# Kernel optimization log

Measured on AMD Instinct MI355X. Metric: run time of the kernel, lower is better.

The kernel has to match this reference:

```python
import jax, jax.numpy as jnp
import numpy as np

N_HEAD = 12
NEG_INF = -10000.0


def setup_inputs() -> dict:
    key = jax.random.key(0)
    k1, k2, k3 = jax.random.split(key, 3)
    B, S, D = 8, 1024, 768
    std = 0.01
    return {
        "hidden_states": jax.random.normal(k1, (B, S, D), dtype=jnp.float32),
        "Wqkv": jax.random.normal(k2, (D, 3 * D), dtype=jnp.float32) * std,
        "bqkv": jnp.zeros((3 * D,), dtype=jnp.float32),
        "Wout": jax.random.normal(k3, (D, D), dtype=jnp.float32) * std,
        "bout": jnp.zeros((D,), dtype=jnp.float32),
    }


def reference(hidden_states, Wqkv, bqkv, Wout, bout):
    B, S, D = hidden_states.shape
    H = N_HEAD
    hd = D // H
    # fused QKV projection
    qkv = hidden_states @ Wqkv + bqkv  # [B,S,3D]
    qkv = qkv.reshape(B, S, 3, H, hd)
    q, k, v = qkv[:, :, 0], qkv[:, :, 1], qkv[:, :, 2]  # [B,S,H,hd]
    q = q.transpose(0, 2, 1, 3)  # [B,H,S,hd]
    k = k.transpose(0, 2, 1, 3)
    v = v.transpose(0, 2, 1, 3)
    scale = 1.0 / jnp.sqrt(jnp.asarray(hd, dtype=hidden_states.dtype))
    scores = jnp.einsum("bhqd,bhkd->bhqk", q, k) * scale  # [B,H,S,S]
    causal = jnp.tril(jnp.ones((S, S), dtype=bool))[None, None]
    scores = jnp.where(causal, scores, jnp.asarray(NEG_INF, scores.dtype))
    probs = jax.nn.softmax(scores, axis=-1)
    # dropout is identity in eval/deterministic mode
    attn = jnp.einsum("bhqk,bhkd->bhqd", probs, v)  # [B,H,S,hd]
    attn = attn.transpose(0, 2, 1, 3).reshape(B, S, D)
    return attn @ Wout + bout
```

## Files before the change

kernel.cpp:

```cpp
#include <hip/hip_runtime.h>
#include <hip/hip_bf16.h>

#define B_   8
#define S_   1024
#define D_   768
#define H_   12
#define HD_  64
#define BS_  (B_*S_)
#define N3_  (3*D_)

typedef __attribute__((ext_vector_type(8))) short short8;
typedef __attribute__((ext_vector_type(4))) float f32x4;

__device__ __forceinline__ short8 ld8(const __hip_bfloat16* p) {
    return *reinterpret_cast<const short8*>(p);
}
__device__ __forceinline__ void st8(__hip_bfloat16* p, short8 v) {
    *reinterpret_cast<short8*>(p) = v;
}
__device__ __forceinline__ f32x4 mfma16(short8 a, short8 b, f32x4 c) {
    return __builtin_amdgcn_mfma_f32_16x16x32_bf16(a, b, c, 0, 0, 0);
}
__device__ __forceinline__ void async16(const __hip_bfloat16* g, __hip_bfloat16* l) {
    __builtin_amdgcn_global_load_lds((const __attribute__((address_space(1))) void*)g,
                                     (__attribute__((address_space(3))) void*)l,
                                     16, 0, 0);
}
__device__ __forceinline__ float fast_exp2(float x) {
#if __has_builtin(__builtin_amdgcn_exp2f)
    return __builtin_amdgcn_exp2f(x);
#else
    return __expf(x * 0.69314718056f);
#endif
}

#define PREP_CAST_BLK 6144
#define PREP_WQKV_BLK 1728
#define PREP_WOUT_BLK 576
__global__ __launch_bounds__(256)
void prep(const float* __restrict__ X, __hip_bfloat16* __restrict__ Xbf,
          const float* __restrict__ Wqkv, __hip_bfloat16* __restrict__ WqkvT,
          const float* __restrict__ Wout, __hip_bfloat16* __restrict__ WoutT) {
    __shared__ float tile[32][33];
    int b = blockIdx.x, tid = threadIdx.x;
    if (b < PREP_CAST_BLK) {
        int i = (b * 256 + tid) * 4;
        float4 v = *reinterpret_cast<const float4*>(X + i);
        __hip_bfloat16 tmp[4];
        tmp[0] = __float2bfloat16(v.x);
        tmp[1] = __float2bfloat16(v.y);
        tmp[2] = __float2bfloat16(v.z);
        tmp[3] = __float2bfloat16(v.w);
        *reinterpret_cast<ushort4*>(Xbf + i) =
            *reinterpret_cast<const ushort4*>(tmp);
        return;
    }
    const float* in; __hip_bfloat16* out; int Rr, Cc, bx, by;
    if (b < PREP_CAST_BLK + PREP_WQKV_BLK) {
        int sub = b - PREP_CAST_BLK;
        bx = sub % (N3_ / 32); by = sub / (N3_ / 32);
        in = Wqkv; out = WqkvT; Rr = D_; Cc = N3_;
    } else {
        int sub = b - PREP_CAST_BLK - PREP_WQKV_BLK;
        bx = sub % (D_ / 32); by = sub / (D_ / 32);
        in = Wout; out = WoutT; Rr = D_; Cc = D_;
    }
    int tx = tid & 31, ty = tid >> 5;
    int c0 = bx * 32, r0 = by * 32;
    for (int i = ty; i < 32; i += 8)
        tile[i][tx] = in[(size_t)(r0 + i) * Cc + c0 + tx];
    __syncthreads();
    for (int i = ty; i < 32; i += 8)
        out[(size_t)(c0 + i) * Rr + r0 + tx] = __float2bfloat16(tile[tx][i]);
}

__global__ __launch_bounds__(256)
void gemm_qkv(const __hip_bfloat16* __restrict__ A,
              const __hip_bfloat16* __restrict__ Bt,
              const float* __restrict__ bqkv,
              __hip_bfloat16* __restrict__ Qb,
              __hip_bfloat16* __restrict__ Kb,
              __hip_bfloat16* __restrict__ Vtb) {
    __shared__ __align__(16) char smem[49152];
    __hip_bfloat16* Ct = (__hip_bfloat16*)smem;

    int tid = threadIdx.x, wave = tid >> 6, lane = tid & 63;
    int ln = lane & 15, quad = lane >> 4;
    int lin = blockIdx.y * 18 + blockIdx.x;
    int work = (lin & 7) * 144 + (lin >> 3);
    int mbb = work / 18, nbb = work % 18;
    int mb = mbb * 128, nb = nbb * 128;
    int wm = (wave >> 1) * 64, wn = (wave & 1) * 64;

    f32x4 acc[4][4];
#pragma unroll
    for (int i = 0; i < 4; ++i)
#pragma unroll
        for (int j = 0; j < 4; ++j) acc[i][j] = (f32x4){0.f, 0.f, 0.f, 0.f};

    auto stage = [&](int k, int bufoff) {
        __hip_bfloat16* Asb = (__hip_bfloat16*)(smem + bufoff);
        __hip_bfloat16* Bsb = Asb + 128 * 32;
#pragma unroll
        for (int it = 0; it < 2; ++it) {
            int c = it * 256 + tid;
            int row = c >> 2, cc = c & 3;
            int csw = cc ^ ((row >> 1) & 3);
            async16(A + (size_t)(mb + row) * D_ + k + csw * 8,
                    Asb + it * 2048 + wave * 512);
            async16(Bt + (size_t)(nb + row) * D_ + k + csw * 8,
                    Bsb + it * 2048 + wave * 512);
        }
    };

    auto compute = [&](int bufoff) {
        __hip_bfloat16* As = (__hip_bfloat16*)(smem + bufoff);
        __hip_bfloat16* Bs = As + 128 * 32;
        short8 a[4], b[4];
#pragma unroll
        for (int i = 0; i < 4; ++i) {
            int row = wm + i * 16 + ln;
            a[i] = ld8(As + row * 32 + ((quad ^ ((row >> 1) & 3)) << 3));
        }
#pragma unroll
        for (int j = 0; j < 4; ++j) {
            int row = wn + j * 16 + ln;
            b[j] = ld8(Bs + row * 32 + ((quad ^ ((row >> 1) & 3)) << 3));
        }
#pragma unroll
        for (int i = 0; i < 4; ++i)
#pragma unroll
            for (int j = 0; j < 4; ++j)
                acc[i][j] = mfma16(a[i], b[j], acc[i][j]);
    };

    stage(0, 0);
    stage(32, 16384);
    int cb = 0;
    for (int k = 0; k < D_ - 32; k += 32) {
        asm volatile("s_waitcnt vmcnt(4)" ::: "memory");
        asm volatile("s_barrier" ::: "memory");
        if (k + 64 < D_) {
            int sb = cb + 32768; if (sb >= 49152) sb -= 49152;
            stage(k + 64, sb);
        }
        compute(cb);
        cb += 16384; if (cb >= 49152) cb = 0;
    }
    asm volatile("s_waitcnt vmcnt(0)" ::: "memory");
    asm volatile("s_barrier" ::: "memory");
    compute(cb);
    __syncthreads();

    int which = nbb / 6;
    int nbr = nb - which * D_;
    float qscale = (which == 0) ? (0.125f * 1.44269504089f) : 1.f;

#pragma unroll
    for (int j = 0; j < 4; ++j) {
        int col = wn + j * 16 + ln;
        float bias = bqkv[nb + col];
#pragma unroll
        for (int i = 0; i < 4; ++i)
#pragma unroll
            for (int r = 0; r < 4; ++r) {
                int row = wm + i * 16 + quad * 4 + r;
                __hip_bfloat16 v = __float2bfloat16((acc[i][j][r] + bias) * qscale);
                if (which != 2) Ct[row * 132 + col] = v;
                else            Ct[col * 132 + row] = v;
            }
    }
    __syncthreads();

    int bb = mb >> 10, sb = mb & 1023;
    if (which != 2) {
        __hip_bfloat16* dst = (which == 0) ? Qb : Kb;
#pragma unroll
        for (int it = 0; it < 8; ++it) {
            int cc = it * 256 + tid;
            int row = cc >> 4, c8 = cc & 15;
            short8 v = ld8(Ct + row * 132 + c8 * 8);
            int gcol = nbr + c8 * 8;
            int h = gcol >> 6, d = gcol & 63;
            int s = sb + row;
            st8(dst + (((size_t)(bb * H_ + h)) * S_ + s) * HD_ + d, v);
        }
    } else {
#pragma unroll
        for (int it = 0; it < 8; ++it) {
            int cc = it * 256 + tid;
            int drow = cc >> 4, s8 = cc & 15;
            short8 v = ld8(Ct + drow * 132 + s8 * 8);
            int gd = nbr + drow;
            int h = gd >> 6, d = gd & 63;
            st8(Vtb + ((size_t)(bb * H_ + h) * HD_ + d) * S_ + sb + s8 * 8, v);
        }
    }
}

__global__ __launch_bounds__(256, 3)
void attn_flash3(const __hip_bfloat16* __restrict__ Q,
                 const __hip_bfloat16* __restrict__ K,
                 const __hip_bfloat16* __restrict__ Vt,
                 __hip_bfloat16* __restrict__ attnbf) {
    __shared__ __hip_bfloat16 Kbuf[2][64 * 64];
    __shared__ __hip_bfloat16 Vbuf[2][64 * 64];
    __shared__ __hip_bfloat16 Pbuf[4][32 * 72];

    int tid = threadIdx.x;
    int wave = tid >> 6, lane = tid & 63;
    int ln = lane & 15, quad = lane >> 4;

    int lin = blockIdx.y * 8 + blockIdx.x;
    int xcd = lin & 7;
    int idx = lin >> 3;
    int jj  = idx & 7;
    int bh  = (idx >> 3) * 8 + xcd;
    int r   = idx >> 5;

    const int TBL1[8] = {4, 5, 6, 7, 0, 1, 2, 3};
    const int TBL2[8] = {6, 4, 2, 0, 7, 5, 3, 1};
    int jp = (r == 0) ? jj : (r == 1) ? TBL1[jj] : TBL2[jj];
    int strip = jp * 2 + (wave >> 1);
    int qrow0 = strip * 64 + (wave & 1) * 32;
    int last_kt = jp * 2 + 1;

    const __hip_bfloat16* Qbh = Q + (size_t)bh * S_ * HD_;
    const __hip_bfloat16* Kbh = K + (size_t)bh * S_ * HD_;
    const __hip_bfloat16* Vbh = Vt + (size_t)bh * HD_ * S_;

    short8 aq[2][2];
#pragma unroll
    for (int rt = 0; rt < 2; ++rt)
#pragma unroll
        for (int ks = 0; ks < 2; ++ks)
            aq[rt][ks] = ld8(Qbh + (size_t)(qrow0 + rt * 16 + ln) * HD_ +
                             ks * 32 + quad * 8);

    f32x4 o[2][4];
    float l_run[2][4];
#pragma unroll
    for (int rt = 0; rt < 2; ++rt)
#pragma unroll
        for (int n = 0; n < 4; ++n) {
            o[rt][n] = (f32x4){0.f, 0.f, 0.f, 0.f};
            l_run[rt][n] = 0.f;
        }

    auto stage = [&](int kt, int buf) {
        const __hip_bfloat16* gK = Kbh + (size_t)kt * 64 * HD_;
#pragma unroll
        for (int it = 0; it < 2; ++it) {
            int p = it * 256 + tid;
            int row = p >> 3;
            int csw = (p & 7) ^ (row & 7);
            async16(gK + row * HD_ + csw * 8,
                    &Kbuf[buf][it * 2048 + wave * 512]);
            async16(Vbh + (size_t)row * S_ + kt * 64 + csw * 8,
                    &Vbuf[buf][it * 2048 + wave * 512]);
        }
    };

    stage(0, 0);
    __syncthreads();
    int cur = 0;

    for (int kt = 0; kt <= last_kt; ++kt) {
        int kbase = kt * 64;
        if (kt < last_kt) stage(kt + 1, cur ^ 1);

        if (kbase <= qrow0 + 31) {
            const __hip_bfloat16* Kc = Kbuf[cur];
            const __hip_bfloat16* Vc = Vbuf[cur];

            f32x4 s[2][4];
#pragma unroll
            for (int rt = 0; rt < 2; ++rt)
#pragma unroll
                for (int j = 0; j < 4; ++j) s[rt][j] = (f32x4){0.f, 0.f, 0.f, 0.f};
            __builtin_amdgcn_s_setprio(1);
#pragma unroll
            for (int j = 0; j < 4; ++j) {
                int row = j * 16 + ln;
#pragma unroll
                for (int ks = 0; ks < 2; ++ks) {
                    short8 bk = ld8(&Kc[row * 64 +
                                        (((ks * 4 + quad) ^ (row & 7)) << 3)]);
#pragma unroll
                    for (int rt = 0; rt < 2; ++rt)
                        s[rt][j] = mfma16(aq[rt][ks], bk, s[rt][j]);
                }
            }
            __builtin_amdgcn_s_setprio(0);

            if (kbase + 63 > qrow0) {
#pragma unroll
                for (int rt = 0; rt < 2; ++rt)
#pragma unroll
                    for (int j = 0; j < 4; ++j) {
                        int key = kbase + j * 16 + ln;
#pragma unroll
                        for (int r2 = 0; r2 < 4; ++r2) {
                            int q = qrow0 + rt * 16 + quad * 4 + r2;
                            if (key > q) s[rt][j][r2] = -INFINITY;
                        }
                    }
            }

#pragma unroll
            for (int rt = 0; rt < 2; ++rt)
#pragma unroll
                for (int j = 0; j < 4; ++j)
#pragma unroll
                    for (int r2 = 0; r2 < 4; ++r2)
                        s[rt][j][r2] = fast_exp2(s[rt][j][r2]);
#pragma unroll
            for (int rt = 0; rt < 2; ++rt)
#pragma unroll
                for (int r2 = 0; r2 < 4; ++r2)
                    l_run[rt][r2] += (s[rt][0][r2] + s[rt][1][r2]) +
                                     (s[rt][2][r2] + s[rt][3][r2]);

#pragma unroll
            for (int rt = 0; rt < 2; ++rt)
#pragma unroll
                for (int j = 0; j < 4; ++j)
#pragma unroll
                    for (int r2 = 0; r2 < 4; ++r2)
                        Pbuf[wave][(rt * 16 + quad * 4 + r2) * 72 + j * 16 + ln] =
                            __float2bfloat16(s[rt][j][r2]);

            short8 ap[2][2];
            asm volatile("s_waitcnt lgkmcnt(15)" ::: "memory");
            __builtin_amdgcn_sched_barrier(0);
#pragma unroll
            for (int ks = 0; ks < 2; ++ks)
                ap[0][ks] = ld8(&Pbuf[wave][(0 * 16 + ln) * 72 +
                                            ks * 32 + quad * 8]);
            asm volatile("s_waitcnt lgkmcnt(0)" ::: "memory");
            __builtin_amdgcn_sched_barrier(0);
#pragma unroll
            for (int ks = 0; ks < 2; ++ks)
                ap[1][ks] = ld8(&Pbuf[wave][(1 * 16 + ln) * 72 +
                                            ks * 32 + quad * 8]);

            __builtin_amdgcn_s_setprio(1);
#pragma unroll
            for (int n = 0; n < 4; ++n) {
                int row = n * 16 + ln;
#pragma unroll
                for (int ks = 0; ks < 2; ++ks) {
                    short8 bv = ld8(&Vc[row * 64 +
                                        (((ks * 4 + quad) ^ (row & 7)) << 3)]);
#pragma unroll
                    for (int rt = 0; rt < 2; ++rt)
                        o[rt][n] = mfma16(ap[rt][ks], bv, o[rt][n]);
                }
            }
            __builtin_amdgcn_s_setprio(0);
        }

        __syncthreads();
        cur ^= 1;
    }

    int bb = bh / H_, h = bh - bb * H_;
#pragma unroll
    for (int rt = 0; rt < 2; ++rt)
#pragma unroll
        for (int r2 = 0; r2 < 4; ++r2) {
            float l = l_run[rt][r2];
            l += __shfl_xor(l, 1);
            l += __shfl_xor(l, 2);
            l += __shfl_xor(l, 4);
            l += __shfl_xor(l, 8);
            float inv = 1.f / l;
            int row = qrow0 + rt * 16 + quad * 4 + r2;
#pragma unroll
            for (int n = 0; n < 4; ++n) {
                int col = h * 64 + n * 16 + ln;
                attnbf[((size_t)bb * S_ + row) * D_ + col] =
                    __float2bfloat16(o[rt][n][r2] * inv);
            }
        }
}

__global__ __launch_bounds__(256, 4)
void gemm_out(const __hip_bfloat16* __restrict__ A,
              const __hip_bfloat16* __restrict__ Bt,
              const float* __restrict__ bias,
              float* __restrict__ Cout) {
    __shared__ __align__(16) char smem[36864];

    int tid = threadIdx.x, wave = tid >> 6, lane = tid & 63;
    int ln = lane & 15, quad = lane >> 4;
    int lin = blockIdx.y * 12 + blockIdx.x;
    int work = (lin & 7) * 96 + (lin >> 3);
    int mbb = work / 12, nbb = work % 12;
    int mb = mbb * 128, nb = nbb * 64;
    int wm = (wave >> 1) * 64, wn = (wave & 1) * 32;

    f32x4 acc[4][2];
#pragma unroll
    for (int i = 0; i < 4; ++i)
#pragma unroll
        for (int j = 0; j < 2; ++j) acc[i][j] = (f32x4){0.f, 0.f, 0.f, 0.f};

    auto stage = [&](int k, int bufoff) {
        __hip_bfloat16* Asb = (__hip_bfloat16*)(smem + bufoff);
        __hip_bfloat16* Bsb = Asb + 128 * 32;
#pragma unroll
        for (int it = 0; it < 2; ++it) {
            int c = it * 256 + tid;
            int row = c >> 2, cc = c & 3;
            int csw = cc ^ ((row >> 1) & 3);
            async16(A + (size_t)(mb + row) * D_ + k + csw * 8,
                    Asb + it * 2048 + wave * 512);
        }
        {
            int c = tid;
            int row = c >> 2, cc = c & 3;
            int csw = cc ^ ((row >> 1) & 3);
            async16(Bt + (size_t)(nb + row) * D_ + k + csw * 8,
                    Bsb + wave * 512);
        }
    };

    auto compute = [&](int bufoff) {
        __hip_bfloat16* As = (__hip_bfloat16*)(smem + bufoff);
        __hip_bfloat16* Bs = As + 128 * 32;
        short8 a[4], b[2];
#pragma unroll
        for (int i = 0; i < 4; ++i) {
            int row = wm + i * 16 + ln;
            a[i] = ld8(As + row * 32 + ((quad ^ ((row >> 1) & 3)) << 3));
        }
#pragma unroll
        for (int j = 0; j < 2; ++j) {
            int row = wn + j * 16 + ln;
            b[j] = ld8(Bs + row * 32 + ((quad ^ ((row >> 1) & 3)) << 3));
        }
#pragma unroll
        for (int i = 0; i < 4; ++i)
#pragma unroll
            for (int j = 0; j < 2; ++j)
                acc[i][j] = mfma16(a[i], b[j], acc[i][j]);
    };

    stage(0, 0);
    stage(32, 12288);
    int cb = 0;
    for (int k = 0; k < D_ - 32; k += 32) {
        asm volatile("s_waitcnt vmcnt(3)" ::: "memory");
        asm volatile("s_barrier" ::: "memory");
        if (k + 64 < D_) {
            int sb = cb + 24576; if (sb >= 36864) sb -= 36864;
            stage(k + 64, sb);
        }
        compute(cb);
        cb += 12288; if (cb >= 36864) cb = 0;
    }
    asm volatile("s_waitcnt vmcnt(0)" ::: "memory");
    asm volatile("s_barrier" ::: "memory");
    compute(cb);

#pragma unroll
    for (int j = 0; j < 2; ++j) {
        int col = nb + wn + j * 16 + ln;
        float bv = bias[col];
#pragma unroll
        for (int i = 0; i < 4; ++i)
#pragma unroll
            for (int r = 0; r < 4; ++r) {
                int row = mb + wm + i * 16 + quad * 4 + r;
                Cout[(size_t)row * D_ + col] = acc[i][j][r] + bv;
            }
    }
}

extern "C" void kernel_launch(void* const* d_in, const int* in_sizes, int n_in,
                              void* d_out, int out_size, void* d_ws, size_t ws_size,
                              hipStream_t stream) {
    const float* X    = (const float*)d_in[0];
    const float* Wqkv = (const float*)d_in[1];
    const float* bqkv = (const float*)d_in[2];
    const float* Wout = (const float*)d_in[3];
    const float* bout = (const float*)d_in[4];
    float* out = (float*)d_out;

    constexpr size_t SZ_XBF   = (size_t)BS_ * D_ * 2;
    constexpr size_t SZ_WQKVT = (size_t)N3_ * D_ * 2;
    constexpr size_t SZ_WOUTT = (size_t)D_ * D_ * 2;
    constexpr size_t SZ_QKV   = (size_t)B_ * H_ * S_ * HD_ * 2;

    char* w = (char*)d_ws;
    __hip_bfloat16* Xbf    = (__hip_bfloat16*)(w);
    __hip_bfloat16* WqkvT  = (__hip_bfloat16*)(w + SZ_XBF);
    __hip_bfloat16* WoutT  = (__hip_bfloat16*)(w + SZ_XBF + SZ_WQKVT);
    __hip_bfloat16* Qb     = (__hip_bfloat16*)(w + SZ_XBF + SZ_WQKVT + SZ_WOUTT);
    __hip_bfloat16* Kb     = (__hip_bfloat16*)(w + SZ_XBF + SZ_WQKVT + SZ_WOUTT + SZ_QKV);
    __hip_bfloat16* Vtb    = (__hip_bfloat16*)(w + SZ_XBF + SZ_WQKVT + SZ_WOUTT + 2*SZ_QKV);
    __hip_bfloat16* attnbf = (__hip_bfloat16*)(w + SZ_XBF + SZ_WQKVT + SZ_WOUTT + 3*SZ_QKV);
    (void)ws_size; (void)in_sizes; (void)n_in; (void)out_size;

    prep<<<PREP_CAST_BLK + PREP_WQKV_BLK + PREP_WOUT_BLK, 256, 0, stream>>>(
        X, Xbf, Wqkv, WqkvT, Wout, WoutT);

    gemm_qkv<<<dim3(N3_ / 128, BS_ / 128), 256, 0, stream>>>(Xbf, WqkvT, bqkv, Qb, Kb, Vtb);

    attn_flash3<<<dim3(8, B_ * H_), 256, 0, stream>>>(Qb, Kb, Vtb, attnbf);

    gemm_out<<<dim3(D_ / 64, BS_ / 128), 256, 0, stream>>>(attnbf, WoutT, bout, out);
}
```

Before: 178.9 us.

## Restructure QKV GEMM into single-wave 64x128 tiles with triple-buffered loads

```diff
diff --git a/kernel.cpp b/kernel.cpp
--- a/kernel.cpp
+++ b/kernel.cpp
@@ -74,110 +74,111 @@
         out[(size_t)(c0 + i) * Rr + r0 + tx] = __float2bfloat16(tile[tx][i]);
 }
 
-__global__ __launch_bounds__(256)
+__global__ __launch_bounds__(64)
 void gemm_qkv(const __hip_bfloat16* __restrict__ A,
               const __hip_bfloat16* __restrict__ Bt,
               const float* __restrict__ bqkv,
               __hip_bfloat16* __restrict__ Qb,
               __hip_bfloat16* __restrict__ Kb,
               __hip_bfloat16* __restrict__ Vtb) {
-    __shared__ __align__(16) char smem[49152];
+    __shared__ __align__(16) char smem[36864];
     __hip_bfloat16* Ct = (__hip_bfloat16*)smem;
 
-    int tid = threadIdx.x, wave = tid >> 6, lane = tid & 63;
+    int lane = threadIdx.x;
     int ln = lane & 15, quad = lane >> 4;
     int lin = blockIdx.y * 18 + blockIdx.x;
-    int work = (lin & 7) * 144 + (lin >> 3);
+    int work = (lin & 7) * 288 + (lin >> 3);
     int mbb = work / 18, nbb = work % 18;
-    int mb = mbb * 128, nb = nbb * 128;
-    int wm = (wave >> 1) * 64, wn = (wave & 1) * 64;
-
-    f32x4 acc[4][4];
+    int mb = mbb * 64, nb = nbb * 128;
+
+    f32x4 acc[4][8];
 #pragma unroll
     for (int i = 0; i < 4; ++i)
 #pragma unroll
-        for (int j = 0; j < 4; ++j) acc[i][j] = (f32x4){0.f, 0.f, 0.f, 0.f};
+        for (int j = 0; j < 8; ++j) acc[i][j] = (f32x4){0.f, 0.f, 0.f, 0.f};
 
     auto stage = [&](int k, int bufoff) {
         __hip_bfloat16* Asb = (__hip_bfloat16*)(smem + bufoff);
-        __hip_bfloat16* Bsb = Asb + 128 * 32;
-#pragma unroll
-        for (int it = 0; it < 2; ++it) {
-            int c = it * 256 + tid;
-            int row = c >> 2, cc = c & 3;
+        __hip_bfloat16* Bsb = Asb + 64 * 32;
+#pragma unroll
+        for (int ld = 0; ld < 4; ++ld) {
+            int q = ld * 64 + lane;
+            int row = q >> 2, cc = q & 3;
             int csw = cc ^ ((row >> 1) & 3);
             async16(A + (size_t)(mb + row) * D_ + k + csw * 8,
-                    Asb + it * 2048 + wave * 512);
+                    Asb + ld * 512);
+        }
+#pragma unroll
+        for (int ld = 0; ld < 8; ++ld) {
+            int q = ld * 64 + lane;
+            int row = q >> 2, cc = q & 3;
+            int csw = cc ^ ((row >> 1) & 3);
             async16(Bt + (size_t)(nb + row) * D_ + k + csw * 8,
-                    Bsb + it * 2048 + wave * 512);
+                    Bsb + ld * 512);
         }
     };
 
     auto compute = [&](int bufoff) {
         __hip_bfloat16* As = (__hip_bfloat16*)(smem + bufoff);
-        __hip_bfloat16* Bs = As + 128 * 32;
-        short8 a[4], b[4];
+        __hip_bfloat16* Bs = As + 64 * 32;
+        short8 a[4], b[8];
 #pragma unroll
         for (int i = 0; i < 4; ++i) {
-            int row = wm + i * 16 + ln;
+            int row = i * 16 + ln;
             a[i] = ld8(As + row * 32 + ((quad ^ ((row >> 1) & 3)) << 3));
         }
 #pragma unroll
-        for (int j = 0; j < 4; ++j) {
-            int row = wn + j * 16 + ln;
+        for (int j = 0; j < 8; ++j) {
+            int row = j * 16 + ln;
             b[j] = ld8(Bs + row * 32 + ((quad ^ ((row >> 1) & 3)) << 3));
         }
 #pragma unroll
         for (int i = 0; i < 4; ++i)
 #pragma unroll
-            for (int j = 0; j < 4; ++j)
+            for (int j = 0; j < 8; ++j)
                 acc[i][j] = mfma16(a[i], b[j], acc[i][j]);
     };
 
     stage(0, 0);
-    stage(32, 16384);
-    int cb = 0;
-    for (int k = 0; k < D_ - 32; k += 32) {
-        asm volatile("s_waitcnt vmcnt(4)" ::: "memory");
-        asm volatile("s_barrier" ::: "memory");
-        if (k + 64 < D_) {
-            int sb = cb + 32768; if (sb >= 49152) sb -= 49152;
-            stage(k + 64, sb);
-        }
-        compute(cb);
-        cb += 16384; if (cb >= 49152) cb = 0;
-    }
-    asm volatile("s_waitcnt vmcnt(0)" ::: "memory");
-    asm volatile("s_barrier" ::: "memory");
-    compute(cb);
-    __syncthreads();
+    stage(32, 12288);
+    for (int t = 0; t < 24; ++t) {
+        if (t < 23) {
+            asm volatile("s_waitcnt vmcnt(12)" ::: "memory");
+        } else {
+            asm volatile("s_waitcnt vmcnt(0)" ::: "memory");
+        }
+        if (t + 2 < 24) {
+            int sb = (t + 2) % 3;
+            stage((t + 2) * 32, sb * 12288);
+        }
+        compute((t % 3) * 12288);
+    }
 
     int which = nbb / 6;
     int nbr = nb - which * D_;
     float qscale = (which == 0) ? (0.125f * 1.44269504089f) : 1.f;
 
 #pragma unroll
-    for (int j = 0; j < 4; ++j) {
-        int col = wn + j * 16 + ln;
+    for (int j = 0; j < 8; ++j) {
+        int col = j * 16 + ln;
         float bias = bqkv[nb + col];
 #pragma unroll
         for (int i = 0; i < 4; ++i)
 #pragma unroll
             for (int r = 0; r < 4; ++r) {
-                int row = wm + i * 16 + quad * 4 + r;
+                int row = i * 16 + quad * 4 + r;
                 __hip_bfloat16 v = __float2bfloat16((acc[i][j][r] + bias) * qscale);
                 if (which != 2) Ct[row * 132 + col] = v;
-                else            Ct[col * 132 + row] = v;
+                else            Ct[col * 68 + row] = v;
             }
     }
-    __syncthreads();
 
     int bb = mb >> 10, sb = mb & 1023;
     if (which != 2) {
         __hip_bfloat16* dst = (which == 0) ? Qb : Kb;
 #pragma unroll
-        for (int it = 0; it < 8; ++it) {
-            int cc = it * 256 + tid;
+        for (int it = 0; it < 16; ++it) {
+            int cc = it * 64 + lane;
             int row = cc >> 4, c8 = cc & 15;
             short8 v = ld8(Ct + row * 132 + c8 * 8);
             int gcol = nbr + c8 * 8;
@@ -187,10 +188,10 @@
         }
     } else {
 #pragma unroll
-        for (int it = 0; it < 8; ++it) {
-            int cc = it * 256 + tid;
-            int drow = cc >> 4, s8 = cc & 15;
-            short8 v = ld8(Ct + drow * 132 + s8 * 8);
+        for (int it = 0; it < 16; ++it) {
+            int cc = it * 64 + lane;
+            int drow = cc >> 3, s8 = cc & 7;
+            short8 v = ld8(Ct + drow * 68 + s8 * 8);
             int gd = nbr + drow;
             int h = gd >> 6, d = gd & 63;
             st8(Vtb + ((size_t)(bb * H_ + h) * HD_ + d) * S_ + sb + s8 * 8, v);
@@ -506,7 +507,7 @@
     prep<<<PREP_CAST_BLK + PREP_WQKV_BLK + PREP_WOUT_BLK, 256, 0, stream>>>(
         X, Xbf, Wqkv, WqkvT, Wout, WoutT);
 
-    gemm_qkv<<<dim3(N3_ / 128, BS_ / 128), 256, 0, stream>>>(Xbf, WqkvT, bqkv, Qb, Kb, Vtb);
+    gemm_qkv<<<dim3(18, BS_ / 64), 64, 0, stream>>>(Xbf, WqkvT, bqkv, Qb, Kb, Vtb);
 
     attn_flash3<<<dim3(8, B_ * H_), 256, 0, stream>>>(Qb, Kb, Vtb, attnbf);
 
```

New measurement: 212.6 us. +18.8%, slower.
